# Kernel optimization log

Hardware: AMD Instinct MI355X
Metric: run time of the kernel (lower is better)

Reference implementation:

```python
import jax, jax.numpy as jnp
import numpy as np
from jax import lax

N, C_IN, L, K, C_OUT, PAD = 16, 64, 8192, 3, 64, 1

def setup_inputs() -> dict:
    key = jax.random.key(0)
    k1, k2, k3 = jax.random.split(key, 3)
    x = jax.random.normal(k1, (N, C_IN, L), dtype=jnp.float32)
    # kaiming normal (relu): std = sqrt(2 / fan_in), fan_in = C_in * kernel_size
    std_off = np.sqrt(2.0 / (C_IN * K)).astype(np.float32)
    w_off = jax.random.normal(k2, (2 * K, C_IN, K), dtype=jnp.float32) * std_off
    b_off = jnp.zeros((2 * K,), dtype=jnp.float32)
    # 1x1 conv: fan_in = C_in * K (kernel_size 1)
    std_w = np.sqrt(2.0 / (C_IN * K)).astype(np.float32)
    w = jax.random.normal(k3, (C_OUT, C_IN * K), dtype=jnp.float32) * std_w
    b = jnp.zeros((C_OUT,), dtype=jnp.float32)
    return {"x": x, "w_off": w_off, "b_off": b_off, "w": w, "b": b}

def reference(x, w_off, b_off, w, b):
    n, c, l = x.shape
    # offset conv: Conv1d(C, 2K, K, stride=1, padding=PAD)
    offsets = lax.conv_general_dilated(
        x, w_off, window_strides=(1,), padding=[(PAD, PAD)],
        dimension_numbers=("NCH", "OIH", "NCH")) + b_off[None, :, None]
    l_out = offsets.shape[2]
    # [N, 2K, L] -> [N, K, 2, L] -> [N, L, K, 2]; only component 0 is used
    off = offsets.reshape(n, K, 2, l_out).transpose(0, 3, 1, 2)[..., 0]  # [N, L, K]
    x_pad = jnp.pad(x, ((0, 0), (0, 0), (PAD, PAD)))
    lp = l + 2 * PAD
    base = jnp.arange(PAD, lp - PAD, dtype=x.dtype)[None, :, None]  # [1, L, 1]
    grid = jnp.clip(base + off, 0.0, lp - 1)                        # [N, L, K]
    left = jnp.floor(grid).astype(jnp.int32)
    right = jnp.minimum(left + 1, lp - 1)
    alpha = grid - left.astype(x.dtype)                              # [N, L, K]
    idx_l = left.reshape(n, -1)
    idx_r = right.reshape(n, -1)
    gather = jax.vmap(lambda xp, i: xp[:, i])  # per-sample gather over length axis
    x_left = gather(x_pad, idx_l).reshape(n, c, l_out, K)
    x_right = gather(x_pad, idx_r).reshape(n, c, l_out, K)
    a = alpha[:, None]  # [N, 1, L, K]
    x_deform = (1.0 - a) * x_left + a * x_right                      # [N, C, L, K]
    # replicate torch's permute(0,3,2,1).view(N, C*K, L) exactly (row-major)
    x_deform = x_deform.transpose(0, 3, 2, 1).reshape(n, c * K, l_out)
    out = jnp.einsum("om,nml->nol", w, x_deform) + b[None, :, None]
    return out
```

## Files before the change

kernel.cpp:

```cpp
#include <hip/hip_runtime.h>
#include <hip/hip_bf16.h>
#include <math.h>

#define NB   16
#define CIN  64
#define LEN  8192
#define LP2  8195
#define COUT 64
#define MSZ  192

typedef float  f32x4  __attribute__((ext_vector_type(4)));
typedef short  bf16x8 __attribute__((ext_vector_type(8)));

static __device__ inline unsigned short f2bf(float f) {
    __hip_bfloat16 h = __float2bfloat16(f);
    return *reinterpret_cast<unsigned short*>(&h);
}

__global__ __launch_bounds__(256) void prep_kernel(
    const float* __restrict__ x, const float* __restrict__ w_off,
    const float* __restrict__ b_off, const float* __restrict__ w,
    float* __restrict__ gbuf, unsigned int* __restrict__ xt32,
    unsigned short* __restrict__ wtf)
{
    int bid = blockIdx.x;
    int tid = threadIdx.x;

    if (bid >= NB * 128) {
        int b = bid - NB * 128;
        int ot = b / 6, ks = b - ot * 6;
        #pragma unroll
        for (int h = 0; h < 2; ++h) {
            int t2 = tid + h * 256;
            int lq = t2 >> 3, s = t2 & 7;
            int o = ot * 16 + (lq & 15);
            int m = ks * 32 + (lq >> 4) * 8 + s;
            wtf[b * 512 + t2] = f2bf(w[o * MSZ + m]);
        }
        return;
    }

    __shared__ float ps[4][3][64];
    __shared__ unsigned int bt[64 * 33];

    int lane = tid & 63;
    int wid  = __builtin_amdgcn_readfirstlane(tid >> 6);
    int n  = bid >> 7;
    int t  = bid & 127;
    int l0 = t << 6;
    int l  = l0 + lane;
    const float* xn = x + (size_t)n * (CIN * LEN);
    bool okm = (l >= 1);
    bool okp = (l < LEN - 1);

    float a0 = 0.f, a1 = 0.f, a2 = 0.f;
    unsigned int pk[8];

    #pragma unroll
    for (int ci = 0; ci < 16; ci += 2) {
        int c0 = (wid << 4) | ci;
        const float* xc0 = xn + (size_t)c0 * LEN;
        const float* xc1 = xc0 + LEN;
        float xm0 = okm ? xc0[l - 1] : 0.f;
        float x00 = xc0[l];
        float xp0 = okp ? xc0[l + 1] : 0.f;
        float xm1 = okm ? xc1[l - 1] : 0.f;
        float x01 = xc1[l];
        float xp1 = okp ? xc1[l + 1] : 0.f;
        const float* wa = w_off + (size_t)c0 * 3;
        const float* wb = wa + 384;
        const float* wc = wa + 768;
        a0 = fmaf(wa[0], xm0, a0); a0 = fmaf(wa[1], x00, a0); a0 = fmaf(wa[2], xp0, a0);
        a0 = fmaf(wa[3], xm1, a0); a0 = fmaf(wa[4], x01, a0); a0 = fmaf(wa[5], xp1, a0);
        a1 = fmaf(wb[0], xm0, a1); a1 = fmaf(wb[1], x00, a1); a1 = fmaf(wb[2], xp0, a1);
        a1 = fmaf(wb[3], xm1, a1); a1 = fmaf(wb[4], x01, a1); a1 = fmaf(wb[5], xp1, a1);
        a2 = fmaf(wc[0], xm0, a2); a2 = fmaf(wc[1], x00, a2); a2 = fmaf(wc[2], xp0, a2);
        a2 = fmaf(wc[3], xm1, a2); a2 = fmaf(wc[4], x01, a2); a2 = fmaf(wc[5], xp1, a2);
        pk[ci >> 1] = ((unsigned int)f2bf(x01) << 16) | f2bf(x00);
    }

    ps[wid][0][lane] = a0;
    ps[wid][1][lane] = a1;
    ps[wid][2][lane] = a2;
    #pragma unroll
    for (int j = 0; j < 8; ++j)
        bt[lane * 33 + (wid << 3) + j] = pk[j];
    __syncthreads();

    if (tid < 192) {
        int k = tid >> 6, ll = tid & 63;
        float s = b_off[2 * k];
        #pragma unroll
        for (int w4 = 0; w4 < 4; ++w4) s += ps[w4][k][ll];
        float g = fminf(fmaxf((float)(l0 + ll + 1) + s, 0.f), 8193.f);
        gbuf[((size_t)n * LEN + l0 + ll) * 3 + k] = g;
    }

    {
        int row = tid >> 2, grp = tid & 3;
        const unsigned int* src = &bt[row * 33 + (grp << 3)];
        uint4 u0, u1;
        u0.x = src[0]; u0.y = src[1]; u0.z = src[2]; u0.w = src[3];
        u1.x = src[4]; u1.y = src[5]; u1.z = src[6]; u1.w = src[7];
        size_t base = ((size_t)n * LP2 + 1 + l0 + row) * 32 + (grp << 3);
        *(uint4*)&xt32[base]     = u0;
        *(uint4*)&xt32[base + 4] = u1;
    }
    if (t == 0   && tid < 32) xt32[((size_t)n * LP2) * 32 + tid] = 0u;
    if (t == 127 && tid < 64) xt32[((size_t)n * LP2 + 8193 + (tid >> 5)) * 32 + (tid & 31)] = 0u;
}

__global__ __launch_bounds__(256) void dconv4_kernel(
    const unsigned short* __restrict__ xt16, const unsigned short* __restrict__ wtf,
    const float* __restrict__ bias, const float* __restrict__ gbuf,
    float* __restrict__ out)
{
    __shared__ __align__(16) int2 meta[MSZ];
    int tid = threadIdx.x;

    int wg  = blockIdx.x;
    int xcd = wg & 7;
    int tt  = wg >> 3;
    int n   = (xcd << 1) | (tt >> 7);
    int p   = tt & 127;

    if (tid < MSZ) {
        int k = tid >> 6, r = tid & 63;
        int l = (r << 7) | p;
        float g  = gbuf[((size_t)n * LEN + l) * 3 + k];
        float fl = floorf(g);
        meta[tid] = make_int2((int)fl, __float_as_int(g - fl));
    }
    __syncthreads();

    int lane = tid & 63;
    int ct   = tid >> 6;
    int g4   = lane >> 4;
    unsigned int c = (unsigned int)(ct * 16 + (lane & 15));
    const unsigned short* xb = xt16 + (size_t)n * LP2 * 64;

    f32x4 acc[4] = {};

    unsigned int xlA[8], xrA[8], xlB[8], xrB[8];
    float alA[8], alB[8];

    #define ISSUE(KS, XL, XR, AL) do {                                       \
        int mb = (KS) * 32 + g4 * 8;                                         \
        int2 mv[8];                                                          \
        _Pragma("unroll")                                                    \
        for (int q = 0; q < 4; ++q)                                          \
            *(int4*)&mv[q * 2] = *(const int4*)&meta[mb + q * 2];            \
        _Pragma("unroll")                                                    \
        for (int s = 0; s < 8; ++s) {                                        \
            unsigned int off = ((unsigned int)mv[s].x << 6) + c;             \
            (XL)[s] = xb[off];                                               \
            (XR)[s] = xb[off + 64];                                          \
            (AL)[s] = __int_as_float(mv[s].y);                               \
        }                                                                    \
    } while (0)

    #define STEP(KS, XL, XR, AL, NXL, NXR, NAL) do {                         \
        if ((KS) < 5) ISSUE((KS) + 1, NXL, NXR, NAL);                        \
        bf16x8 afrag;                                                        \
        _Pragma("unroll")                                                    \
        for (int s = 0; s < 8; ++s) {                                        \
            float a  = (AL)[s];                                              \
            float vl = __uint_as_float((XL)[s] << 16);                       \
            float vr = __uint_as_float((XR)[s] << 16);                       \
            afrag[s] = (short)f2bf(fmaf(a, vr - vl, vl));                    \
        }                                                                    \
        _Pragma("unroll")                                                    \
        for (int ot = 0; ot < 4; ++ot) {                                     \
            bf16x8 bfrag = *(const bf16x8*)&wtf[(size_t)(((ot * 6 + (KS)) << 6) + lane) << 3]; \
            acc[ot] = __builtin_amdgcn_mfma_f32_16x16x32_bf16(afrag, bfrag, acc[ot], 0, 0, 0); \
        }                                                                    \
    } while (0)

    ISSUE(0, xlA, xrA, alA);
    STEP(0, xlA, xrA, alA, xlB, xrB, alB);
    STEP(1, xlB, xrB, alB, xlA, xrA, alA);
    STEP(2, xlA, xrA, alA, xlB, xrB, alB);
    STEP(3, xlB, xrB, alB, xlA, xrA, alA);
    STEP(4, xlA, xrA, alA, xlB, xrB, alB);
    STEP(5, xlB, xrB, alB, xlA, xrA, alA);

    #undef ISSUE
    #undef STEP

    int q0 = (p << 6) + ct * 16 + g4 * 4;
    #pragma unroll
    for (int ot = 0; ot < 4; ++ot) {
        int o = ot * 16 + (lane & 15);
        float bb = bias[o];
        float4 r4;
        r4.x = acc[ot][0] + bb;
        r4.y = acc[ot][1] + bb;
        r4.z = acc[ot][2] + bb;
        r4.w = acc[ot][3] + bb;
        *(float4*)&out[((size_t)n * COUT + o) * LEN + q0] = r4;
    }
}

extern "C" void kernel_launch(void* const* d_in, const int* in_sizes, int n_in,
                              void* d_out, int out_size, void* d_ws, size_t ws_size,
                              hipStream_t stream) {
    const float* x     = (const float*)d_in[0];
    const float* w_off = (const float*)d_in[1];
    const float* b_off = (const float*)d_in[2];
    const float* w     = (const float*)d_in[3];
    const float* b     = (const float*)d_in[4];
    float* out = (float*)d_out;

    const size_t GBUF_B = (size_t)NB * LEN * 3 * sizeof(float);
    const size_t WTF_B  = (size_t)MSZ * COUT * sizeof(short);
    float*          gbuf = (float*)d_ws;
    unsigned short* wtf  = (unsigned short*)((char*)d_ws + GBUF_B);
    unsigned int*   xt32 = (unsigned int*)((char*)d_ws + GBUF_B + WTF_B);
    unsigned short* xt16 = (unsigned short*)xt32;

    prep_kernel<<<NB * 128 + 24, 256, 0, stream>>>(x, w_off, b_off, w, gbuf, xt32, wtf);
    dconv4_kernel<<<NB * 128, 256, 0, stream>>>(xt16, wtf, b, gbuf, out);
}
```

Baseline: 41.89 us.

## Stage interpolated gather rows in swizzled LDS via 16-byte vector loads

Result: faster. 37.44 us (-10.6%).

```diff
diff --git a/kernel.cpp b/kernel.cpp
--- a/kernel.cpp
+++ b/kernel.cpp
@@ -110,11 +110,12 @@
     if (t == 127 && tid < 64) xt32[((size_t)n * LP2 + 8193 + (tid >> 5)) * 32 + (tid & 31)] = 0u;
 }
 
-__global__ __launch_bounds__(256) void dconv4_kernel(
+__global__ __launch_bounds__(256) void dconv6_kernel(
     const unsigned short* __restrict__ xt16, const unsigned short* __restrict__ wtf,
     const float* __restrict__ bias, const float* __restrict__ gbuf,
     float* __restrict__ out)
 {
+    __shared__ unsigned short Bl[MSZ * 64];
     __shared__ __align__(16) int2 meta[MSZ];
     int tid = threadIdx.x;
 
@@ -133,59 +134,58 @@
     }
     __syncthreads();
 
+    const unsigned short* xb = xt16 + (size_t)n * LP2 * 64;
+
+    #pragma unroll
+    for (int j = 0; j < 6; ++j) {
+        int task = tid + (j << 8);
+        int m  = task >> 3;
+        int ch = task & 7;
+        int2 mv = meta[m];
+        float a = __int_as_float(mv.y);
+        const unsigned short* rl = xb + ((size_t)(unsigned)mv.x << 6) + (ch << 3);
+        uint4 vl4 = *(const uint4*)rl;
+        uint4 vr4 = *(const uint4*)(rl + 64);
+        const unsigned int* vl = (const unsigned int*)&vl4;
+        const unsigned int* vr = (const unsigned int*)&vr4;
+        unsigned int ov[4];
+        #pragma unroll
+        for (int q = 0; q < 4; ++q) {
+            float l0 = __uint_as_float(vl[q] << 16);
+            float l1 = __uint_as_float(vl[q] & 0xffff0000u);
+            float r0 = __uint_as_float(vr[q] << 16);
+            float r1 = __uint_as_float(vr[q] & 0xffff0000u);
+            float b0 = fmaf(a, r0 - l0, l0);
+            float b1 = fmaf(a, r1 - l1, l1);
+            ov[q] = ((unsigned int)f2bf(b1) << 16) | f2bf(b0);
+        }
+        int dst = (m << 6) + ((ch << 3) ^ (((m >> 3) & 3) << 4));
+        *(uint4*)&Bl[dst] = *(const uint4*)ov;
+    }
+    __syncthreads();
+
     int lane = tid & 63;
     int ct   = tid >> 6;
     int g4   = lane >> 4;
-    unsigned int c = (unsigned int)(ct * 16 + (lane & 15));
-    const unsigned short* xb = xt16 + (size_t)n * LP2 * 64;
+    int c    = (ct << 4) | (lane & 15);
 
     f32x4 acc[4] = {};
 
-    unsigned int xlA[8], xrA[8], xlB[8], xrB[8];
-    float alA[8], alB[8];
-
-    #define ISSUE(KS, XL, XR, AL) do {                                       \
-        int mb = (KS) * 32 + g4 * 8;                                         \
-        int2 mv[8];                                                          \
-        _Pragma("unroll")                                                    \
-        for (int q = 0; q < 4; ++q)                                          \
-            *(int4*)&mv[q * 2] = *(const int4*)&meta[mb + q * 2];            \
-        _Pragma("unroll")                                                    \
-        for (int s = 0; s < 8; ++s) {                                        \
-            unsigned int off = ((unsigned int)mv[s].x << 6) + c;             \
-            (XL)[s] = xb[off];                                               \
-            (XR)[s] = xb[off + 64];                                          \
-            (AL)[s] = __int_as_float(mv[s].y);                               \
-        }                                                                    \
-    } while (0)
-
-    #define STEP(KS, XL, XR, AL, NXL, NXR, NAL) do {                         \
-        if ((KS) < 5) ISSUE((KS) + 1, NXL, NXR, NAL);                        \
-        bf16x8 afrag;                                                        \
-        _Pragma("unroll")                                                    \
-        for (int s = 0; s < 8; ++s) {                                        \
-            float a  = (AL)[s];                                              \
-            float vl = __uint_as_float((XL)[s] << 16);                       \
-            float vr = __uint_as_float((XR)[s] << 16);                       \
-            afrag[s] = (short)f2bf(fmaf(a, vr - vl, vl));                    \
-        }                                                                    \
-        _Pragma("unroll")                                                    \
-        for (int ot = 0; ot < 4; ++ot) {                                     \
-            bf16x8 bfrag = *(const bf16x8*)&wtf[(size_t)(((ot * 6 + (KS)) << 6) + lane) << 3]; \
-            acc[ot] = __builtin_amdgcn_mfma_f32_16x16x32_bf16(afrag, bfrag, acc[ot], 0, 0, 0); \
-        }                                                                    \
-    } while (0)
-
-    ISSUE(0, xlA, xrA, alA);
-    STEP(0, xlA, xrA, alA, xlB, xrB, alB);
-    STEP(1, xlB, xrB, alB, xlA, xrA, alA);
-    STEP(2, xlA, xrA, alA, xlB, xrB, alB);
-    STEP(3, xlB, xrB, alB, xlA, xrA, alA);
-    STEP(4, xlA, xrA, alA, xlB, xrB, alB);
-    STEP(5, xlB, xrB, alB, xlA, xrA, alA);
-
-    #undef ISSUE
-    #undef STEP
+    #pragma unroll
+    for (int ks = 0; ks < 6; ++ks) {
+        int mb = ks * 32 + (g4 << 3);
+        int cx = c ^ ((((unsigned)(mb >> 3)) & 3) << 4);
+        bf16x8 afrag;
+        #pragma unroll
+        for (int s = 0; s < 8; ++s)
+            afrag[s] = (short)Bl[((mb + s) << 6) + cx];
+
+        #pragma unroll
+        for (int ot = 0; ot < 4; ++ot) {
+            bf16x8 bfrag = *(const bf16x8*)&wtf[(size_t)(((ot * 6 + ks) << 6) + lane) << 3];
+            acc[ot] = __builtin_amdgcn_mfma_f32_16x16x32_bf16(afrag, bfrag, acc[ot], 0, 0, 0);
+        }
+    }
 
     int q0 = (p << 6) + ct * 16 + g4 * 4;
     #pragma unroll
@@ -219,5 +219,5 @@
     unsigned short* xt16 = (unsigned short*)xt32;
 
     prep_kernel<<<NB * 128 + 24, 256, 0, stream>>>(x, w_off, b_off, w, gbuf, xt32, wtf);
-    dconv4_kernel<<<NB * 128, 256, 0, stream>>>(xt16, wtf, b, gbuf, out);
-}
+    dconv6_kernel<<<NB * 128, 256, 0, stream>>>(xt16, wtf, b, gbuf, out);
+}
```
